# Kernel optimization log

Measured on AMD Instinct MI355X. Metric: run time of the kernel, lower is better.

## Reference

```python
import jax, jax.numpy as jnp
import numpy as np

HOP, NA, AL = 240, 16, 32  # hop_length, num_atoms, atom_length (HOP >= AL, so placed atoms never overlap)
B, C, T = 32, 128, 4096
AUDIO_LEN = (T - 1) * HOP + AL  # 982832


def conv1d(x, w, b=None, padding=0, groups=1):
    out = jax.lax.conv_general_dilated(
        x, w, window_strides=(1,), padding=[(padding, padding)],
        dimension_numbers=('NCH', 'OIH', 'NCH'), feature_group_count=groups)
    if b is not None:
        out = out + b[None, :, None]
    return out


def setup_inputs() -> dict:
    key = jax.random.key(0)
    ks = jax.random.split(key, 20)
    n = lambda k, shp, s=0.1: (jax.random.normal(k, shp, jnp.float32) * s)
    return {
        'condition': jax.random.normal(ks[0], (B, C, T), jnp.float32),
        'audio_length': AUDIO_LEN,
        # envelope_net: dw-sep(128->64), dw-sep(64->32), conv(32->1)
        'dw1_w': n(ks[1], (128, 1, 3)), 'dw1_b': n(ks[2], (128,)),
        'pw1_w': n(ks[3], (64, 128, 1)), 'pw1_b': n(ks[4], (64,)),
        'dw2_w': n(ks[5], (64, 1, 3)), 'dw2_b': n(ks[6], (64,)),
        'pw2_w': n(ks[7], (32, 64, 1)), 'pw2_b': n(ks[8], (32,)),
        'env_w': n(ks[9], (1, 32, 3)), 'env_b': n(ks[10], (1,)),
        # envelope_smoother: 7-tap box filter, no bias
        'smooth_w': jnp.ones((1, 1, 7), jnp.float32) / 7.0,
        # atom_selector: dw-sep(128->64), conv(64->16)
        'sdw_w': n(ks[11], (128, 1, 3)), 'sdw_b': n(ks[12], (128,)),
        'spw_w': n(ks[13], (64, 128, 1)), 'spw_b': n(ks[14], (64,)),
        'sel_w': n(ks[15], (16, 64, 3)), 'sel_b': n(ks[16], (16,)),
        # transient dictionary (also the atom_placer weights after _sync)
        'atoms': jax.random.normal(ks[17], (NA, AL), jnp.float32),
    }


def _fwd(condition, audio_length, dw1_w, dw1_b, pw1_w, pw1_b, dw2_w, dw2_b,
         pw2_w, pw2_b, env_w, env_b, smooth_w, sdw_w, sdw_b, spw_w, spw_b,
         sel_w, sel_b, atoms):
    b, c, t = condition.shape  # static Python ints
    req = (audio_length - AL) // HOP + 1
    if (req - 1) * HOP + AL != audio_length:
        req = (audio_length - AL) // HOP + 2
    if req > t:
        condition = jnp.pad(condition, ((0, 0), (0, 0), (0, req - t)))
        t = req
    lrelu = lambda x: jax.nn.leaky_relu(x, 0.1)
    # envelope_net
    h = lrelu(conv1d(conv1d(condition, dw1_w, dw1_b, 1, c), pw1_w, pw1_b))
    h = lrelu(conv1d(conv1d(h, dw2_w, dw2_b, 1, 64), pw2_w, pw2_b))
    envelope = jax.nn.sigmoid(conv1d(h, env_w, env_b, 1))  # [B,1,T]
    # atom_selector
    s = lrelu(conv1d(conv1d(condition, sdw_w, sdw_b, 1, c), spw_w, spw_b))
    logits = conv1d(s, sel_w, sel_b, 1)  # [B,NA,T]
    # sparse top-k softmax over atom dim, fully vectorized (no python loops)
    k = min(3, NA)
    lt = jnp.transpose(logits, (0, 2, 1))            # [B,T,NA]
    vals, idx = jax.lax.top_k(lt, k)                 # [B,T,k]
    sm = jax.nn.softmax(vals, axis=-1)               # softmax over top-k only
    oh = jax.nn.one_hot(idx, NA, dtype=sm.dtype)     # [B,T,k,NA]
    weights = jnp.einsum('btk,btka->bat', sm, oh)    # scatter back -> [B,NA,T]
    # atom_placer: ConvTranspose1d(stride=HOP, kernel=AL); since HOP>=AL frames never overlap,
    # so transposed conv == per-frame atom mix placed at t*HOP
    frames = jnp.einsum('bat,al->btl', weights, atoms)      # [B,T,AL]
    frames = jnp.pad(frames, ((0, 0), (0, 0), (0, HOP - AL)))
    placed = frames.reshape(b, t * HOP)[:, :(t - 1) * HOP + AL][:, None, :]
    pl = placed.shape[2]
    if pl > audio_length:
        placed = placed[:, :, :audio_length]
    elif pl < audio_length:
        placed = jnp.pad(placed, ((0, 0), (0, 0), (0, audio_length - pl)))
    lout = placed.shape[2]
    # F.interpolate(mode='nearest'): src = floor(dst * in/out)
    nn_idx = np.floor(np.arange(lout) * (t / lout)).astype(np.int32)
    env_up = envelope[:, :, nn_idx]                  # [B,1,audio_length]
    env_up = conv1d(env_up, smooth_w, None, 3)
    return (placed * env_up)[:, 0, :]                # [B,audio_length]


def reference(condition, audio_length, dw1_w, dw1_b, pw1_w, pw1_b, dw2_w,
              dw2_b, pw2_w, pw2_b, env_w, env_b, smooth_w, sdw_w, sdw_b,
              spw_w, spw_b, sel_w, sel_b, atoms):
    return _fwd(condition, audio_length, dw1_w, dw1_b, pw1_w, pw1_b, dw2_w,
                dw2_b, pw2_w, pw2_b, env_w, env_b, smooth_w, sdw_w, sdw_b,
                spw_w, spw_b, sel_w, sel_b, atoms)
```

## Files before the change

kernel.cpp:

```cpp
#include <hip/hip_runtime.h>
#include <math.h>

#define NB 32
#define NC 128
#define NT 4096
#define LTOT 982832
#define BT 64

__device__ __forceinline__ float lrelu_(float x) { return x > 0.0f ? x : 0.1f * x; }
__device__ __forceinline__ int swz_(int row, int ch) {
    return ((ch & ~3) ^ ((row & 56) >> 1)) | (ch & 3);
}

__global__ __launch_bounds__(256)
void k_wt(const float* __restrict__ pw1w, const float* __restrict__ spww,
          float* __restrict__ wt1, float* __restrict__ wt2)
{
    const int i = blockIdx.x * 256 + threadIdx.x;
    if (i < 64 * 128) {
        const int o = i >> 7, c = i & 127;
        wt1[c * 64 + o] = pw1w[i];
        wt2[c * 64 + o] = spww[i];
    }
}

__global__ __launch_bounds__(256, 4)
void k_stage1r(const float* __restrict__ cond,
               const float* __restrict__ dww, const float* __restrict__ dwb,
               const float* __restrict__ wt,  const float* __restrict__ pwb,
               float* __restrict__ out64)
{
    const int tid  = threadIdx.x;
    const int lane = tid & 63;
    const int wv   = tid >> 6;
    const int cgrp = wv >> 1;
    const int so0  = __builtin_amdgcn_readfirstlane((wv & 1) * 32);

    const int col = blockIdx.x * 128 + cgrp * 64 + lane;
    const int b   = col >> 12;
    const int t   = col & (NT - 1);
    const float* xp = cond + (size_t)b * NC * NT + t;
    const bool gm = (t >= 1);
    const bool gp = (t + 1 < NT);

    float acc[32];
    #pragma unroll
    for (int o = 0; o < 32; ++o) acc[o] = 0.0f;

    #pragma unroll 2
    for (int c = 0; c < NC; ++c) {
        const float xm = gm ? xp[-1] : 0.0f;
        const float xc = xp[0];
        const float xq = gp ? xp[1] : 0.0f;
        const float h  = fmaf(dww[c * 3 + 0], xm,
                         fmaf(dww[c * 3 + 1], xc,
                         fmaf(dww[c * 3 + 2], xq, dwb[c])));
        const float* wr = wt + (c << 6) + so0;
        #pragma unroll
        for (int og = 0; og < 4; ++og) {
            const float4 wa = *(const float4*)(wr + og * 8);
            const float4 wb = *(const float4*)(wr + og * 8 + 4);
            acc[og * 8 + 0] = fmaf(wa.x, h, acc[og * 8 + 0]);
            acc[og * 8 + 1] = fmaf(wa.y, h, acc[og * 8 + 1]);
            acc[og * 8 + 2] = fmaf(wa.z, h, acc[og * 8 + 2]);
            acc[og * 8 + 3] = fmaf(wa.w, h, acc[og * 8 + 3]);
            acc[og * 8 + 4] = fmaf(wb.x, h, acc[og * 8 + 4]);
            acc[og * 8 + 5] = fmaf(wb.y, h, acc[og * 8 + 5]);
            acc[og * 8 + 6] = fmaf(wb.z, h, acc[og * 8 + 6]);
            acc[og * 8 + 7] = fmaf(wb.w, h, acc[og * 8 + 7]);
        }
        xp += NT;
    }

    float* op = out64 + (size_t)col * 64 + so0;
    #pragma unroll
    for (int g = 0; g < 8; ++g) {
        const float4 bb = *(const float4*)&pwb[so0 + g * 4];
        float4 r;
        r.x = lrelu_(acc[g * 4 + 0] + bb.x);
        r.y = lrelu_(acc[g * 4 + 1] + bb.y);
        r.z = lrelu_(acc[g * 4 + 2] + bb.z);
        r.w = lrelu_(acc[g * 4 + 3] + bb.w);
        *(float4*)(op + g * 4) = r;
    }
}

__global__ __launch_bounds__(256)
void k_env2(const float* __restrict__ y1,
            const float* __restrict__ dw2w, const float* __restrict__ dw2b,
            const float* __restrict__ pw2w, const float* __restrict__ pw2b,
            const float* __restrict__ envw, const float* __restrict__ envb,
            float* __restrict__ envout)
{
    __shared__ float Y1T[70 * 68];
    __shared__ float H2T[68 * 68];
    float* Y2T = Y1T;

    const int tid = threadIdx.x;
    const int b   = blockIdx.y;
    const int t0  = blockIdx.x * BT;

    for (int i = tid; i < 70 * 64; i += 256) {
        int j = i >> 6, o = i & 63;
        int t = t0 - 3 + j;
        Y1T[j * 68 + o] = (t >= 0 && t < NT) ? y1[((size_t)b * NT + t) * 64 + o] : 0.0f;
    }
    __syncthreads();

    {
        const int o = tid & 63;
        const int g = tid >> 6;
        const float d0 = dw2w[o * 3 + 0], d1 = dw2w[o * 3 + 1], d2 = dw2w[o * 3 + 2], db = dw2b[o];
        float y[19];
        #pragma unroll
        for (int k = 0; k < 19; ++k) y[k] = Y1T[(g * 17 + k) * 68 + o];
        #pragma unroll
        for (int i = 0; i < 17; ++i) {
            int jj = g * 17 + i;
            H2T[jj * 68 + swz_(jj, o)] = fmaf(d0, y[i], fmaf(d1, y[i + 1], fmaf(d2, y[i + 2], db)));
        }
    }
    __syncthreads();

    {
        const int v  = tid & 63;
        const int wu = __builtin_amdgcn_readfirstlane(threadIdx.x >> 6);
        const float* wbase = pw2w + wu * 8 * 64;
        float acc[8], acc2[8];
        #pragma unroll
        for (int q = 0; q < 8; ++q) { acc[q] = 0.0f; acc2[q] = 0.0f; }
        const int r1 = v + 1;
        const int r2 = (v < 2) ? v + 65 : v + 1;
        const float* h1 = &H2T[r1 * 68]; const int x1 = (r1 & 56) >> 1;
        const float* h2 = &H2T[r2 * 68]; const int x2 = (r2 & 56) >> 1;
        #pragma unroll 2
        for (int cc = 0; cc < 64; cc += 4) {
            const float4 a  = *(const float4*)&h1[cc ^ x1];
            const float4 c2 = *(const float4*)&h2[cc ^ x2];
            #pragma unroll
            for (int q = 0; q < 8; ++q) {
                const float4 wv = *(const float4*)&wbase[q * 64 + cc];
                acc[q]  = fmaf(wv.x, a.x,  fmaf(wv.y, a.y,  fmaf(wv.z, a.z,  fmaf(wv.w, a.w,  acc[q]))));
                acc2[q] = fmaf(wv.x, c2.x, fmaf(wv.y, c2.y, fmaf(wv.z, c2.z, fmaf(wv.w, c2.w, acc2[q]))));
            }
        }
        const int t1 = t0 - 1 + v;
        const bool ok1 = (t1 >= 0 && t1 < NT);
        #pragma unroll
        for (int q = 0; q < 8; ++q) {
            const float bq = pw2b[wu * 8 + q];
            Y2T[v * 37 + wu * 8 + q] = ok1 ? lrelu_(acc[q] + bq) : 0.0f;
        }
        if (v < 2) {
            const int ve = v + 64;
            const int t2 = t0 - 1 + ve;
            const bool ok2 = (t2 >= 0 && t2 < NT);
            #pragma unroll
            for (int q = 0; q < 8; ++q) {
                const float bq = pw2b[wu * 8 + q];
                Y2T[ve * 37 + wu * 8 + q] = ok2 ? lrelu_(acc2[q] + bq) : 0.0f;
            }
        }
    }
    __syncthreads();

    {
        const int j  = tid >> 2;
        const int cp = tid & 3;
        float a = 0.0f;
        #pragma unroll
        for (int d = 0; d < 3; ++d) {
            const float* yr = &Y2T[(j + d) * 37 + cp * 8];
            #pragma unroll
            for (int k = 0; k < 8; ++k)
                a = fmaf(envw[(cp * 8 + k) * 3 + d], yr[k], a);
        }
        a += __shfl_xor(a, 1);
        a += __shfl_xor(a, 2);
        if (cp == 0) {
            const float z = a + envb[0];
            envout[(size_t)b * NT + t0 + j] = 1.0f / (1.0f + expf(-z));
        }
    }
}

__global__ __launch_bounds__(256)
void k_sel2(const float* __restrict__ ss,
            const float* __restrict__ selw, const float* __restrict__ selb,
            float4* __restrict__ selout)
{
    __shared__ float SST[66 * 68];
    __shared__ float Lg[16 * 64];

    const int tid = threadIdx.x;
    const int b   = blockIdx.y;
    const int t0  = blockIdx.x * BT;

    for (int i = tid; i < 66 * 64; i += 256) {
        int j = i >> 6, o = i & 63;
        int t = t0 - 1 + j;
        SST[j * 68 + swz_(j, o)] = (t >= 0 && t < NT) ? ss[((size_t)b * NT + t) * 64 + o] : 0.0f;
    }
    __syncthreads();

    {
        const int v  = tid & 63;
        const int wu = __builtin_amdgcn_readfirstlane(threadIdx.x >> 6);
        float acc[4] = {0.0f, 0.0f, 0.0f, 0.0f};
        const float* r0 = &SST[(v + 0) * 68]; const int x0 = ((v + 0) & 56) >> 1;
        const float* r1 = &SST[(v + 1) * 68]; const int x1 = ((v + 1) & 56) >> 1;
        const float* r2 = &SST[(v + 2) * 68]; const int x2 = ((v + 2) & 56) >> 1;
        #pragma unroll 2
        for (int cc = 0; cc < 64; cc += 4) {
            const float4 s0 = *(const float4*)&r0[cc ^ x0];
            const float4 s1 = *(const float4*)&r1[cc ^ x1];
            const float4 s2 = *(const float4*)&r2[cc ^ x2];
            #pragma unroll
            for (int q = 0; q < 4; ++q) {
                const float* wr = selw + (size_t)(wu * 4 + q) * 192 + cc * 3;
                const float4 wA = *(const float4*)&wr[0];
                const float4 wB = *(const float4*)&wr[4];
                const float4 wC = *(const float4*)&wr[8];
                acc[q] = fmaf(wA.x, s0.x, acc[q]); acc[q] = fmaf(wA.y, s1.x, acc[q]); acc[q] = fmaf(wA.z, s2.x, acc[q]);
                acc[q] = fmaf(wA.w, s0.y, acc[q]); acc[q] = fmaf(wB.x, s1.y, acc[q]); acc[q] = fmaf(wB.y, s2.y, acc[q]);
                acc[q] = fmaf(wB.z, s0.z, acc[q]); acc[q] = fmaf(wB.w, s1.z, acc[q]); acc[q] = fmaf(wC.x, s2.z, acc[q]);
                acc[q] = fmaf(wC.y, s0.w, acc[q]); acc[q] = fmaf(wC.z, s1.w, acc[q]); acc[q] = fmaf(wC.w, s2.w, acc[q]);
            }
        }
        #pragma unroll
        for (int q = 0; q < 4; ++q)
            Lg[(wu * 4 + q) * 64 + v] = acc[q] + selb[wu * 4 + q];
    }
    __syncthreads();

    if (tid < 64) {
        const int jt = tid;
        float v[16];
        #pragma unroll
        for (int a = 0; a < 16; ++a) v[a] = Lg[a * 64 + jt];
        int i0 = 0; float m0 = v[0];
        #pragma unroll
        for (int a = 1; a < 16; ++a) if (v[a] > m0) { m0 = v[a]; i0 = a; }
        v[i0] = -INFINITY;
        int i1 = 0; float m1 = v[0];
        #pragma unroll
        for (int a = 1; a < 16; ++a) if (v[a] > m1) { m1 = v[a]; i1 = a; }
        v[i1] = -INFINITY;
        int i2 = 0; float m2 = v[0];
        #pragma unroll
        for (int a = 1; a < 16; ++a) if (v[a] > m2) { m2 = v[a]; i2 = a; }
        float e1 = expf(m1 - m0), e2 = expf(m2 - m0);
        float s = 1.0f + e1 + e2;
        float4 r;
        r.x = 1.0f / s;
        r.y = e1 / s;
        r.z = e2 / s;
        r.w = (float)(i0 | (i1 << 4) | (i2 << 8));
        selout[(size_t)b * NT + t0 + jt] = r;
    }
}

__global__ __launch_bounds__(256)
void k_out(const float* __restrict__ env,
           const float4* __restrict__ sel,
           const float* __restrict__ atoms,
           const float* __restrict__ smw,
           float* __restrict__ out)
{
    __shared__ float at[512];
    __shared__ float ps[8];
    const int tid = threadIdx.x;
    for (int i = tid; i < 512; i += 256) at[i] = atoms[i];
    if (tid == 0) {
        float s = 0.0f;
        #pragma unroll
        for (int c = 0; c < 7; ++c) { ps[c] = s; s += smw[c]; }
        ps[7] = s;
    }
    __syncthreads();

    const int fid  = blockIdx.x * 4 + (tid >> 6);
    const int b    = fid >> 12;
    const int t    = fid & 4095;
    const int lane = tid & 63;
    const int base = b * LTOT + t * 240;

    if (lane < 8) {
        const float4 sv = sel[fid];
        const int p  = (int)(sv.w + 0.5f);
        const int i0 = p & 15, i1 = (p >> 4) & 15, i2 = (p >> 8) & 15;
        const int j0 = lane * 4;
        float r[4];
        if (t == 0 || t == NT - 1) {
            #pragma unroll
            for (int q = 0; q < 4; ++q) {
                const int j = j0 + q;
                const float fv = sv.x * at[i0 * 32 + j] + sv.y * at[i1 * 32 + j] + sv.z * at[i2 * 32 + j];
                const int ip = t * 240 + j;
                float es = 0.0f;
                #pragma unroll
                for (int d = -3; d <= 3; ++d) {
                    const int ii = ip + d;
                    if (ii >= 0 && ii < LTOT) {
                        const int nn = (int)((double)ii * (4096.0 / 982832.0));
                        es = fmaf(smw[d + 3], env[b * NT + nn], es);
                    }
                }
                r[q] = fv * es;
            }
        } else {
            const int ip0 = t * 240;
            const int ii0 = ip0 - 3;
            const int n0  = (int)((double)ii0 * (4096.0 / 982832.0));
            int K = ((n0 + 1) * 61427 + 255) >> 8;
            if ((int)((double)(K - 1) * (4096.0 / 982832.0)) > n0) --K;
            else if ((int)((double)K * (4096.0 / 982832.0)) == n0) ++K;
            const float e0 = env[b * NT + n0];
            const int   n1 = (n0 + 1 < NT) ? n0 + 1 : NT - 1;
            const float e1 = env[b * NT + n1];
            const float pst = ps[7];
            #pragma unroll
            for (int q = 0; q < 4; ++q) {
                const int j = j0 + q;
                const int ip = ip0 + j;
                int c = K - (ip - 3);
                c = (c < 0) ? 0 : ((c > 7) ? 7 : c);
                const float A  = ps[c];
                const float es = fmaf(A, e0 - e1, pst * e1);
                const float fv = sv.x * at[i0 * 32 + j] + sv.y * at[i1 * 32 + j] + sv.z * at[i2 * 32 + j];
                r[q] = fv * es;
            }
        }
        *(float4*)(out + base + j0) = make_float4(r[0], r[1], r[2], r[3]);
    } else if (lane < 60) {
        const int idx = t * 240 + lane * 4;
        if (idx + 4 <= LTOT) {
            *(float4*)(out + base + lane * 4) = make_float4(0.0f, 0.0f, 0.0f, 0.0f);
        }
    }
}

extern "C" void kernel_launch(void* const* d_in, const int* in_sizes, int n_in,
                              void* d_out, int out_size, void* d_ws, size_t ws_size,
                              hipStream_t stream)
{
    const float* cond  = (const float*)d_in[0];
    const float* dw1w  = (const float*)d_in[2];
    const float* dw1b  = (const float*)d_in[3];
    const float* pw1w  = (const float*)d_in[4];
    const float* pw1b  = (const float*)d_in[5];
    const float* dw2w  = (const float*)d_in[6];
    const float* dw2b  = (const float*)d_in[7];
    const float* pw2w  = (const float*)d_in[8];
    const float* pw2b  = (const float*)d_in[9];
    const float* envw  = (const float*)d_in[10];
    const float* envb  = (const float*)d_in[11];
    const float* smw   = (const float*)d_in[12];
    const float* sdww  = (const float*)d_in[13];
    const float* sdwb  = (const float*)d_in[14];
    const float* spww  = (const float*)d_in[15];
    const float* spwb  = (const float*)d_in[16];
    const float* selw  = (const float*)d_in[17];
    const float* selb  = (const float*)d_in[18];
    const float* atoms = (const float*)d_in[19];
    float* out = (float*)d_out;

    float*  envbuf = (float*)d_ws;
    float4* selbuf = (float4*)((char*)d_ws + 524288);
    float*  y1buf  = (float*)((char*)d_ws + 524288 + 2097152);
    float*  wt1    = (float*)((char*)d_ws + 524288 + 2097152 + 33554432);
    float*  wt2    = wt1 + 64 * 128;

    k_wt<<<32, 256, 0, stream>>>(pw1w, spww, wt1, wt2);

    dim3 g(NT / BT, NB);
    const int gr = (NB * NT) / 128;
    k_stage1r<<<gr, 256, 0, stream>>>(cond, dw1w, dw1b, wt1, pw1b, y1buf);
    k_env2<<<g, 256, 0, stream>>>(y1buf, dw2w, dw2b, pw2w, pw2b, envw, envb, envbuf);
    k_stage1r<<<gr, 256, 0, stream>>>(cond, sdww, sdwb, wt2, spwb, y1buf);
    k_sel2<<<g, 256, 0, stream>>>(y1buf, selw, selb, selbuf);
    k_out<<<(NB * NT) / 4, 256, 0, stream>>>(envbuf, selbuf, atoms, smw, out);
}
```

Baseline: 206.8 us.

## Fuse envelope and selector stage-1 convs into dual-output kernels sharing input reads

```diff
diff --git a/kernel.cpp b/kernel.cpp
--- a/kernel.cpp
+++ b/kernel.cpp
@@ -21,6 +21,172 @@
         const int o = i >> 7, c = i & 127;
         wt1[c * 64 + o] = pw1w[i];
         wt2[c * 64 + o] = spww[i];
+    }
+}
+
+__global__ __launch_bounds__(256, 2)
+void k_stage1d(const float* __restrict__ cond,
+               const float* __restrict__ dw1w, const float* __restrict__ dw1b,
+               const float* __restrict__ wt1,  const float* __restrict__ pw1b,
+               const float* __restrict__ sdww, const float* __restrict__ sdwb,
+               const float* __restrict__ wt2,  const float* __restrict__ spwb,
+               float* __restrict__ y1out, float* __restrict__ ssout)
+{
+    const int col = blockIdx.x * 256 + threadIdx.x;
+    const int b   = col >> 12;
+    const int t   = col & (NT - 1);
+    const float* xp0 = cond + (size_t)b * NC * NT + t;
+    const bool gm = (t >= 1);
+    const bool gp = (t + 1 < NT);
+
+    float accA[32], accB[32];
+    #pragma unroll
+    for (int o = 0; o < 32; ++o) { accA[o] = 0.0f; accB[o] = 0.0f; }
+
+    #pragma unroll 1
+    for (int cc = 0; cc < NC; cc += 4) {
+        float xm[4], xc[4], xq[4];
+        #pragma unroll
+        for (int u = 0; u < 4; ++u) {
+            const float* row = xp0 + (size_t)(cc + u) * NT;
+            xm[u] = gm ? row[-1] : 0.0f;
+            xc[u] = row[0];
+            xq[u] = gp ? row[1] : 0.0f;
+        }
+        #pragma unroll
+        for (int u = 0; u < 4; ++u) {
+            const int c = cc + u;
+            const float hA = fmaf(dw1w[c * 3 + 0], xm[u],
+                             fmaf(dw1w[c * 3 + 1], xc[u],
+                             fmaf(dw1w[c * 3 + 2], xq[u], dw1b[c])));
+            const float hB = fmaf(sdww[c * 3 + 0], xm[u],
+                             fmaf(sdww[c * 3 + 1], xc[u],
+                             fmaf(sdww[c * 3 + 2], xq[u], sdwb[c])));
+            const float* wA = wt1 + (c << 6);
+            const float* wB = wt2 + (c << 6);
+            #pragma unroll
+            for (int og = 0; og < 8; ++og) {
+                const float4 wa = *(const float4*)(wA + og * 4);
+                accA[og * 4 + 0] = fmaf(wa.x, hA, accA[og * 4 + 0]);
+                accA[og * 4 + 1] = fmaf(wa.y, hA, accA[og * 4 + 1]);
+                accA[og * 4 + 2] = fmaf(wa.z, hA, accA[og * 4 + 2]);
+                accA[og * 4 + 3] = fmaf(wa.w, hA, accA[og * 4 + 3]);
+            }
+            #pragma unroll
+            for (int og = 0; og < 8; ++og) {
+                const float4 wb = *(const float4*)(wB + og * 4);
+                accB[og * 4 + 0] = fmaf(wb.x, hB, accB[og * 4 + 0]);
+                accB[og * 4 + 1] = fmaf(wb.y, hB, accB[og * 4 + 1]);
+                accB[og * 4 + 2] = fmaf(wb.z, hB, accB[og * 4 + 2]);
+                accB[og * 4 + 3] = fmaf(wb.w, hB, accB[og * 4 + 3]);
+            }
+        }
+    }
+
+    float* opA = y1out + (size_t)col * 64;
+    float* opB = ssout + (size_t)col * 64;
+    #pragma unroll
+    for (int g = 0; g < 8; ++g) {
+        const float4 ba = *(const float4*)&pw1b[g * 4];
+        float4 r;
+        r.x = lrelu_(accA[g * 4 + 0] + ba.x);
+        r.y = lrelu_(accA[g * 4 + 1] + ba.y);
+        r.z = lrelu_(accA[g * 4 + 2] + ba.z);
+        r.w = lrelu_(accA[g * 4 + 3] + ba.w);
+        *(float4*)(opA + g * 4) = r;
+    }
+    #pragma unroll
+    for (int g = 0; g < 8; ++g) {
+        const float4 bs = *(const float4*)&spwb[g * 4];
+        float4 r;
+        r.x = lrelu_(accB[g * 4 + 0] + bs.x);
+        r.y = lrelu_(accB[g * 4 + 1] + bs.y);
+        r.z = lrelu_(accB[g * 4 + 2] + bs.z);
+        r.w = lrelu_(accB[g * 4 + 3] + bs.w);
+        *(float4*)(opB + g * 4) = r;
+    }
+}
+
+__global__ __launch_bounds__(256, 2)
+void k_stage1d_hi(const float* __restrict__ cond,
+                  const float* __restrict__ dw1w, const float* __restrict__ dw1b,
+                  const float* __restrict__ wt1,  const float* __restrict__ pw1b,
+                  const float* __restrict__ sdww, const float* __restrict__ sdwb,
+                  const float* __restrict__ wt2,  const float* __restrict__ spwb,
+                  float* __restrict__ y1out, float* __restrict__ ssout)
+{
+    const int col = blockIdx.x * 256 + threadIdx.x;
+    const int b   = col >> 12;
+    const int t   = col & (NT - 1);
+    const float* xp0 = cond + (size_t)b * NC * NT + t;
+    const bool gm = (t >= 1);
+    const bool gp = (t + 1 < NT);
+
+    float accA[32], accB[32];
+    #pragma unroll
+    for (int o = 0; o < 32; ++o) { accA[o] = 0.0f; accB[o] = 0.0f; }
+
+    #pragma unroll 1
+    for (int cc = 0; cc < NC; cc += 4) {
+        float xm[4], xc[4], xq[4];
+        #pragma unroll
+        for (int u = 0; u < 4; ++u) {
+            const float* row = xp0 + (size_t)(cc + u) * NT;
+            xm[u] = gm ? row[-1] : 0.0f;
+            xc[u] = row[0];
+            xq[u] = gp ? row[1] : 0.0f;
+        }
+        #pragma unroll
+        for (int u = 0; u < 4; ++u) {
+            const int c = cc + u;
+            const float hA = fmaf(dw1w[c * 3 + 0], xm[u],
+                             fmaf(dw1w[c * 3 + 1], xc[u],
+                             fmaf(dw1w[c * 3 + 2], xq[u], dw1b[c])));
+            const float hB = fmaf(sdww[c * 3 + 0], xm[u],
+                             fmaf(sdww[c * 3 + 1], xc[u],
+                             fmaf(sdww[c * 3 + 2], xq[u], sdwb[c])));
+            const float* wA = wt1 + (c << 6) + 32;
+            const float* wB = wt2 + (c << 6) + 32;
+            #pragma unroll
+            for (int og = 0; og < 8; ++og) {
+                const float4 wa = *(const float4*)(wA + og * 4);
+                accA[og * 4 + 0] = fmaf(wa.x, hA, accA[og * 4 + 0]);
+                accA[og * 4 + 1] = fmaf(wa.y, hA, accA[og * 4 + 1]);
+                accA[og * 4 + 2] = fmaf(wa.z, hA, accA[og * 4 + 2]);
+                accA[og * 4 + 3] = fmaf(wa.w, hA, accA[og * 4 + 3]);
+            }
+            #pragma unroll
+            for (int og = 0; og < 8; ++og) {
+                const float4 wb = *(const float4*)(wB + og * 4);
+                accB[og * 4 + 0] = fmaf(wb.x, hB, accB[og * 4 + 0]);
+                accB[og * 4 + 1] = fmaf(wb.y, hB, accB[og * 4 + 1]);
+                accB[og * 4 + 2] = fmaf(wb.z, hB, accB[og * 4 + 2]);
+                accB[og * 4 + 3] = fmaf(wb.w, hB, accB[og * 4 + 3]);
+            }
+        }
+    }
+
+    float* opA = y1out + (size_t)col * 64 + 32;
+    float* opB = ssout + (size_t)col * 64 + 32;
+    #pragma unroll
+    for (int g = 0; g < 8; ++g) {
+        const float4 ba = *(const float4*)&pw1b[32 + g * 4];
+        float4 r;
+        r.x = lrelu_(accA[g * 4 + 0] + ba.x);
+        r.y = lrelu_(accA[g * 4 + 1] + ba.y);
+        r.z = lrelu_(accA[g * 4 + 2] + ba.z);
+        r.w = lrelu_(accA[g * 4 + 3] + ba.w);
+        *(float4*)(opA + g * 4) = r;
+    }
+    #pragma unroll
+    for (int g = 0; g < 8; ++g) {
+        const float4 bs = *(const float4*)&spwb[32 + g * 4];
+        float4 r;
+        r.x = lrelu_(accB[g * 4 + 0] + bs.x);
+        r.y = lrelu_(accB[g * 4 + 1] + bs.y);
+        r.z = lrelu_(accB[g * 4 + 2] + bs.z);
+        r.w = lrelu_(accB[g * 4 + 3] + bs.w);
+        *(float4*)(opB + g * 4) = r;
     }
 }
 
@@ -365,19 +531,41 @@
     const float* atoms = (const float*)d_in[19];
     float* out = (float*)d_out;
 
+    const size_t SZ_ENV = 524288;
+    const size_t SZ_SEL = 2097152;
+    const size_t SZ_Y1  = 33554432;
+    const size_t SZ_WT  = 65536;
+
     float*  envbuf = (float*)d_ws;
-    float4* selbuf = (float4*)((char*)d_ws + 524288);
-    float*  y1buf  = (float*)((char*)d_ws + 524288 + 2097152);
-    float*  wt1    = (float*)((char*)d_ws + 524288 + 2097152 + 33554432);
-    float*  wt2    = wt1 + 64 * 128;
-
-    k_wt<<<32, 256, 0, stream>>>(pw1w, spww, wt1, wt2);
+    float4* selbuf = (float4*)((char*)d_ws + SZ_ENV);
+    float*  y1buf  = (float*)((char*)d_ws + SZ_ENV + SZ_SEL);
 
     dim3 g(NT / BT, NB);
-    const int gr = (NB * NT) / 128;
-    k_stage1r<<<gr, 256, 0, stream>>>(cond, dw1w, dw1b, wt1, pw1b, y1buf);
-    k_env2<<<g, 256, 0, stream>>>(y1buf, dw2w, dw2b, pw2w, pw2b, envw, envb, envbuf);
-    k_stage1r<<<gr, 256, 0, stream>>>(cond, sdww, sdwb, wt2, spwb, y1buf);
-    k_sel2<<<g, 256, 0, stream>>>(y1buf, selw, selb, selbuf);
+
+    if (ws_size >= SZ_ENV + SZ_SEL + 2 * SZ_Y1 + SZ_WT) {
+        float* ssbuf = (float*)((char*)d_ws + SZ_ENV + SZ_SEL + SZ_Y1);
+        float* wt1   = (float*)((char*)d_ws + SZ_ENV + SZ_SEL + 2 * SZ_Y1);
+        float* wt2   = wt1 + 64 * 128;
+
+        k_wt<<<32, 256, 0, stream>>>(pw1w, spww, wt1, wt2);
+        const int gd = (NB * NT) / 256;
+        k_stage1d<<<gd, 256, 0, stream>>>(cond, dw1w, dw1b, wt1, pw1b,
+                                          sdww, sdwb, wt2, spwb, y1buf, ssbuf);
+        k_stage1d_hi<<<gd, 256, 0, stream>>>(cond, dw1w, dw1b, wt1, pw1b,
+                                             sdww, sdwb, wt2, spwb, y1buf, ssbuf);
+        k_env2<<<g, 256, 0, stream>>>(y1buf, dw2w, dw2b, pw2w, pw2b, envw, envb, envbuf);
+        k_sel2<<<g, 256, 0, stream>>>(ssbuf, selw, selb, selbuf);
+    } else {
+        float* wt1 = (float*)((char*)d_ws + SZ_ENV + SZ_SEL + SZ_Y1);
+        float* wt2 = wt1 + 64 * 128;
+
+        k_wt<<<32, 256, 0, stream>>>(pw1w, spww, wt1, wt2);
+        const int gr = (NB * NT) / 128;
+        k_stage1r<<<gr, 256, 0, stream>>>(cond, dw1w, dw1b, wt1, pw1b, y1buf);
+        k_env2<<<g, 256, 0, stream>>>(y1buf, dw2w, dw2b, pw2w, pw2b, envw, envb, envbuf);
+        k_stage1r<<<gr, 256, 0, stream>>>(cond, sdww, sdwb, wt2, spwb, y1buf);
+        k_sel2<<<g, 256, 0, stream>>>(y1buf, selw, selb, selbuf);
+    }
+
     k_out<<<(NB * NT) / 4, 256, 0, stream>>>(envbuf, selbuf, atoms, smw, out);
 }
```

Result: slower. 333.1 us (+61.1%).
